# Optimization experiments

Measured on AMD Instinct MI355X. Metric: run time of the kernel, lower is better.

## Reference

```python
import jax, jax.numpy as jnp
import numpy as np

H = 128
B = 1024  # must equal seq_len per the original module's quirk
S = 1024


def setup_inputs() -> dict:
    key = jax.random.key(0)
    k1, k2, k3, k4, k5 = jax.random.split(key, 5)
    hidden = jax.random.normal(k1, (B, H), dtype=jnp.float32)
    encoder_outputs = jax.random.normal(k2, (B, S, H), dtype=jnp.float32)
    # nn.Linear(2H, H): weight [H, 2H], bias [H]
    W = jax.random.normal(k3, (H, 2 * H), dtype=jnp.float32) * (1.0 / np.sqrt(2 * H))
    b = jax.random.normal(k4, (H,), dtype=jnp.float32) * 0.01
    # self.v = nn.Parameter(torch.rand(hidden_size))
    v = jax.random.uniform(k5, (H,), dtype=jnp.float32)
    return {"hidden": hidden, "encoder_outputs": encoder_outputs, "W": W, "b": b, "v": v}


def reference(hidden, encoder_outputs, W, b, v):
    # cat((hidden_rep, enc), dim=2) @ W.T == hidden @ W[:, :H].T + enc @ W[:, H:].T
    Wh, We = W[:, :H], W[:, H:]
    eh = hidden @ Wh.T                                  # [B, H]
    ee = jnp.einsum('bsh,oh->bso', encoder_outputs, We)  # [B, S, H]
    energy = jnp.tanh(eh[:, None, :] + ee + b)           # [B, S, H]
    scores = jnp.einsum('bsh,h->bs', energy, v)          # v^T . energy (bmm)
    return jax.nn.softmax(scores, axis=1)
```

## Files before the change

kernel.cpp:

```cpp
#include <hip/hip_runtime.h>
#include <hip/hip_bf16.h>

namespace {

constexpr int HD = 128;
constexpr int SB = 1024;
constexpr int BB = 1024;

typedef __attribute__((ext_vector_type(4)))  float          f32x4;
typedef __attribute__((ext_vector_type(16))) float          f32x16;
typedef __attribute__((ext_vector_type(8)))  __bf16         bf16x8;
typedef __attribute__((ext_vector_type(8)))  unsigned short u16x8;
typedef __attribute__((ext_vector_type(4)))  unsigned short u16x4;

__device__ __forceinline__ float fast_tanh(float x) {
  float e = __expf(2.0f * x);
  return 1.0f - 2.0f * __builtin_amdgcn_rcpf(e + 1.0f);
}

}

extern "C" __global__ __launch_bounds__(512, 1)
void attn_fused(const float* __restrict__ hidden,
                const float* __restrict__ enc,
                const float* __restrict__ W,
                const float* __restrict__ bias,
                const float* __restrict__ vvec,
                float* __restrict__ out)
{
  __shared__ unsigned short WeHi[HD * HD];
  __shared__ unsigned short WeLo[HD * HD];
  __shared__ float hid[HD];
  __shared__ float ehb[HD];
  __shared__ float sc[SB];
  __shared__ float red[16];

  const int b    = blockIdx.x;
  const int tid  = threadIdx.x;
  const int lane = tid & 63;
  const int wv   = tid >> 6;
  const int l31  = lane & 31;
  const int hi   = lane >> 5;

  if (tid < 32)
    ((f32x4*)hid)[tid] = ((const f32x4*)(hidden + (size_t)b * HD))[tid];
  __syncthreads();

  if (tid < HD) {
    const float* wr = W + (size_t)tid * (2 * HD);
    float acc = bias[tid];
    #pragma unroll
    for (int h = 0; h < HD; h += 4) {
      f32x4 wq = *(const f32x4*)(wr + h);
      acc += hid[h]     * wq[0];
      acc += hid[h + 1] * wq[1];
      acc += hid[h + 2] * wq[2];
      acc += hid[h + 3] * wq[3];
    }
    ehb[tid] = acc;
  } else {
    for (int e = tid - HD; e < (HD * HD / 4); e += 384) {
      const int o  = e >> 5;
      const int h4 = (e & 31) << 2;
      f32x4 x = *(const f32x4*)(W + (size_t)o * (2 * HD) + HD + h4);
      const int g   = (h4 >> 3) ^ (o & 15);
      const int idx = o * HD + g * 8 + (h4 & 7);
      u16x4 hv, lv;
      #pragma unroll
      for (int j = 0; j < 4; ++j) {
        float xx = x[j];
        __bf16 hb = (__bf16)xx;
        float hf = (float)hb;
        __bf16 lb = (__bf16)(xx - hf);
        hv[j] = __builtin_bit_cast(unsigned short, hb);
        lv[j] = __builtin_bit_cast(unsigned short, lb);
      }
      *(u16x4*)&WeHi[idx] = hv;
      *(u16x4*)&WeLo[idx] = lv;
    }
  }
  __syncthreads();

  const float vt0 = vvec[l31],      vt1 = vvec[32 + l31];
  const float vt2 = vvec[64 + l31], vt3 = vvec[96 + l31];
  const float et0 = ehb[l31],       et1 = ehb[32 + l31];
  const float et2 = ehb[64 + l31],  et3 = ehb[96 + l31];

  for (int c = 0; c < 4; ++c) {
    const int s0 = c * 256 + wv * 32;
    const float* ap = enc + ((size_t)b * SB + (s0 + l31)) * HD + hi * 8;

    f32x4 araw[16];
    #pragma unroll
    for (int ks = 0; ks < 8; ++ks) {
      araw[2 * ks]     = *(const f32x4*)(ap + ks * 16);
      araw[2 * ks + 1] = *(const f32x4*)(ap + ks * 16 + 4);
    }

    f32x16 acc0 = {}, acc1 = {}, acc2 = {}, acc3 = {};

    #pragma unroll
    for (int ks = 0; ks < 8; ++ks) {
      bf16x8 ah, al;
      #pragma unroll
      for (int j = 0; j < 8; ++j) {
        float xx = (j < 4) ? araw[2 * ks][j] : araw[2 * ks + 1][j - 4];
        __bf16 hb = (__bf16)xx;
        ah[j] = hb;
        al[j] = (__bf16)(xx - (float)hb);
      }
      const int gsw = ((ks * 2 + hi) ^ (l31 & 15)) * 8;

#define DO_TILE(ACC, T)                                                      \
      {                                                                      \
        const int bi = ((T) * 32 + l31) * HD + gsw;                          \
        bf16x8 bh = __builtin_bit_cast(bf16x8, *(const u16x8*)&WeHi[bi]);    \
        bf16x8 bl = __builtin_bit_cast(bf16x8, *(const u16x8*)&WeLo[bi]);    \
        ACC = __builtin_amdgcn_mfma_f32_32x32x16_bf16(ah, bh, ACC, 0, 0, 0); \
        ACC = __builtin_amdgcn_mfma_f32_32x32x16_bf16(al, bh, ACC, 0, 0, 0); \
        ACC = __builtin_amdgcn_mfma_f32_32x32x16_bf16(ah, bl, ACC, 0, 0, 0); \
      }

      DO_TILE(acc0, 0)
      DO_TILE(acc1, 1)
      DO_TILE(acc2, 2)
      DO_TILE(acc3, 3)
#undef DO_TILE
    }

    float ps[16];
    #pragma unroll
    for (int r = 0; r < 16; ++r) {
      ps[r] = vt0 * fast_tanh(acc0[r] + et0)
            + vt1 * fast_tanh(acc1[r] + et1)
            + vt2 * fast_tanh(acc2[r] + et2)
            + vt3 * fast_tanh(acc3[r] + et3);
    }
    #pragma unroll
    for (int d = 1; d <= 16; d <<= 1) {
      #pragma unroll
      for (int r = 0; r < 16; ++r)
        ps[r] += __shfl_xor(ps[r], d, 64);
    }
    if (l31 == 0) {
      #pragma unroll
      for (int r = 0; r < 16; ++r) {
        const int row = (r & 3) + 8 * (r >> 2) + 4 * hi;
        sc[s0 + row] = ps[r];
      }
    }
  }
  __syncthreads();

  const float x0 = sc[tid];
  const float x1 = sc[tid + 512];
  float m = fmaxf(x0, x1);
  #pragma unroll
  for (int d = 32; d >= 1; d >>= 1) m = fmaxf(m, __shfl_xor(m, d, 64));
  if (lane == 0) red[wv] = m;
  __syncthreads();
  float M = red[0];
  #pragma unroll
  for (int i = 1; i < 8; ++i) M = fmaxf(M, red[i]);
  const float e0 = __expf(x0 - M);
  const float e1 = __expf(x1 - M);
  float s2 = e0 + e1;
  #pragma unroll
  for (int d = 32; d >= 1; d >>= 1) s2 += __shfl_xor(s2, d, 64);
  if (lane == 0) red[8 + wv] = s2;
  __syncthreads();
  float T = 0.0f;
  #pragma unroll
  for (int i = 0; i < 8; ++i) T += red[8 + i];
  const float inv = 1.0f / T;
  out[(size_t)b * SB + tid]       = e0 * inv;
  out[(size_t)b * SB + 512 + tid] = e1 * inv;
}

extern "C" void kernel_launch(void* const* d_in, const int* in_sizes, int n_in,
                              void* d_out, int out_size, void* d_ws, size_t ws_size,
                              hipStream_t stream) {
  const float* hidden = (const float*)d_in[0];
  const float* enc    = (const float*)d_in[1];
  const float* W      = (const float*)d_in[2];
  const float* bias   = (const float*)d_in[3];
  const float* vvec   = (const float*)d_in[4];
  float* out = (float*)d_out;
  (void)in_sizes; (void)n_in; (void)out_size; (void)d_ws; (void)ws_size;
  attn_fused<<<dim3(BB), dim3(512), 0, stream>>>(hidden, enc, W, bias, vvec, out);
}
```

Baseline: 890.4 us.

## Switch energy GEMM from 32x32x16 to 16x16x32 MFMA tiles

Restructures the per-chunk GEMM to use 16x16x32 bf16 MFMA instructions, processing 16 sequence rows per wave over 8 chunks instead of 32 rows over 4, with 8 output tiles per wave. Accumulators shrink from four 16-wide vectors to eight 4-wide vectors, the cross-lane reduction drops from 5 shuffle rounds on 16 values to 4 rounds on 4 values, and the launch-bounds min-blocks hint is removed. The aim is lower register pressure and cheaper epilogue reduction, at the cost of smaller tiles per load and more loop iterations.

```diff
diff --git a/kernel.cpp b/kernel.cpp
--- a/kernel.cpp
+++ b/kernel.cpp
@@ -8,7 +8,6 @@
 constexpr int BB = 1024;
 
 typedef __attribute__((ext_vector_type(4)))  float          f32x4;
-typedef __attribute__((ext_vector_type(16))) float          f32x16;
 typedef __attribute__((ext_vector_type(8)))  __bf16         bf16x8;
 typedef __attribute__((ext_vector_type(8)))  unsigned short u16x8;
 typedef __attribute__((ext_vector_type(4)))  unsigned short u16x4;
@@ -20,7 +19,7 @@
 
 }
 
-extern "C" __global__ __launch_bounds__(512, 1)
+extern "C" __global__ __launch_bounds__(512)
 void attn_fused(const float* __restrict__ hidden,
                 const float* __restrict__ enc,
                 const float* __restrict__ W,
@@ -39,8 +38,8 @@
   const int tid  = threadIdx.x;
   const int lane = tid & 63;
   const int wv   = tid >> 6;
-  const int l31  = lane & 31;
-  const int hi   = lane >> 5;
+  const int l15  = lane & 15;
+  const int hi4  = lane >> 4;
 
   if (tid < 32)
     ((f32x4*)hid)[tid] = ((const f32x4*)(hidden + (size_t)b * HD))[tid];
@@ -81,73 +80,66 @@
   }
   __syncthreads();
 
-  const float vt0 = vvec[l31],      vt1 = vvec[32 + l31];
-  const float vt2 = vvec[64 + l31], vt3 = vvec[96 + l31];
-  const float et0 = ehb[l31],       et1 = ehb[32 + l31];
-  const float et2 = ehb[64 + l31],  et3 = ehb[96 + l31];
+  float vt[8], et[8];
+  #pragma unroll
+  for (int T = 0; T < 8; ++T) {
+    vt[T] = vvec[T * 16 + l15];
+    et[T] = ehb[T * 16 + l15];
+  }
 
-  for (int c = 0; c < 4; ++c) {
-    const int s0 = c * 256 + wv * 32;
-    const float* ap = enc + ((size_t)b * SB + (s0 + l31)) * HD + hi * 8;
+  for (int c = 0; c < 8; ++c) {
+    const int s0 = c * 128 + wv * 16;
+    const float* ap = enc + ((size_t)b * SB + (s0 + l15)) * HD + hi4 * 8;
 
-    f32x4 araw[16];
+    bf16x8 ah[4], al[4];
     #pragma unroll
-    for (int ks = 0; ks < 8; ++ks) {
-      araw[2 * ks]     = *(const f32x4*)(ap + ks * 16);
-      araw[2 * ks + 1] = *(const f32x4*)(ap + ks * 16 + 4);
+    for (int ks = 0; ks < 4; ++ks) {
+      f32x4 r0 = *(const f32x4*)(ap + ks * 32);
+      f32x4 r1 = *(const f32x4*)(ap + ks * 32 + 4);
+      #pragma unroll
+      for (int j = 0; j < 8; ++j) {
+        float xx = (j < 4) ? r0[j] : r1[j - 4];
+        __bf16 hb = (__bf16)xx;
+        ah[ks][j] = hb;
+        al[ks][j] = (__bf16)(xx - (float)hb);
+      }
     }
 
-    f32x16 acc0 = {}, acc1 = {}, acc2 = {}, acc3 = {};
+    f32x4 acc[8] = {};
 
     #pragma unroll
-    for (int ks = 0; ks < 8; ++ks) {
-      bf16x8 ah, al;
+    for (int ks = 0; ks < 4; ++ks) {
+      const int slot = (((ks * 4 + hi4) ^ l15)) * 8;
       #pragma unroll
-      for (int j = 0; j < 8; ++j) {
-        float xx = (j < 4) ? araw[2 * ks][j] : araw[2 * ks + 1][j - 4];
-        __bf16 hb = (__bf16)xx;
-        ah[j] = hb;
-        al[j] = (__bf16)(xx - (float)hb);
+      for (int T = 0; T < 8; ++T) {
+        const int bi = (T * 16 + l15) * HD + slot;
+        bf16x8 bh = __builtin_bit_cast(bf16x8, *(const u16x8*)&WeHi[bi]);
+        bf16x8 bl = __builtin_bit_cast(bf16x8, *(const u16x8*)&WeLo[bi]);
+        acc[T] = __builtin_amdgcn_mfma_f32_16x16x32_bf16(ah[ks], bh, acc[T], 0, 0, 0);
+        acc[T] = __builtin_amdgcn_mfma_f32_16x16x32_bf16(al[ks], bh, acc[T], 0, 0, 0);
+        acc[T] = __builtin_amdgcn_mfma_f32_16x16x32_bf16(ah[ks], bl, acc[T], 0, 0, 0);
       }
-      const int gsw = ((ks * 2 + hi) ^ (l31 & 15)) * 8;
-
-#define DO_TILE(ACC, T)                                                      \
-      {                                                                      \
-        const int bi = ((T) * 32 + l31) * HD + gsw;                          \
-        bf16x8 bh = __builtin_bit_cast(bf16x8, *(const u16x8*)&WeHi[bi]);    \
-        bf16x8 bl = __builtin_bit_cast(bf16x8, *(const u16x8*)&WeLo[bi]);    \
-        ACC = __builtin_amdgcn_mfma_f32_32x32x16_bf16(ah, bh, ACC, 0, 0, 0); \
-        ACC = __builtin_amdgcn_mfma_f32_32x32x16_bf16(al, bh, ACC, 0, 0, 0); \
-        ACC = __builtin_amdgcn_mfma_f32_32x32x16_bf16(ah, bl, ACC, 0, 0, 0); \
-      }
-
-      DO_TILE(acc0, 0)
-      DO_TILE(acc1, 1)
-      DO_TILE(acc2, 2)
-      DO_TILE(acc3, 3)
-#undef DO_TILE
     }
 
-    float ps[16];
+    float ps[4];
     #pragma unroll
-    for (int r = 0; r < 16; ++r) {
-      ps[r] = vt0 * fast_tanh(acc0[r] + et0)
-            + vt1 * fast_tanh(acc1[r] + et1)
-            + vt2 * fast_tanh(acc2[r] + et2)
-            + vt3 * fast_tanh(acc3[r] + et3);
+    for (int r = 0; r < 4; ++r) {
+      float s = 0.0f;
+      #pragma unroll
+      for (int T = 0; T < 8; ++T)
+        s += vt[T] * fast_tanh(acc[T][r] + et[T]);
+      ps[r] = s;
     }
     #pragma unroll
-    for (int d = 1; d <= 16; d <<= 1) {
+    for (int d = 1; d <= 8; d <<= 1) {
       #pragma unroll
-      for (int r = 0; r < 16; ++r)
+      for (int r = 0; r < 4; ++r)
         ps[r] += __shfl_xor(ps[r], d, 64);
     }
-    if (l31 == 0) {
+    if (l15 == 0) {
       #pragma unroll
-      for (int r = 0; r < 16; ++r) {
-        const int row = (r & 3) + 8 * (r >> 2) + 4 * hi;
-        sc[s0 + row] = ps[r];
-      }
+      for (int r = 0; r < 4; ++r)
+        sc[s0 + hi4 * 4 + r] = ps[r];
     }
   }
   __syncthreads();
```

Result: slower. 990.2 us (+11.2%).
